# Performance work log

Hardware: AMD Instinct MI355X
Metric: run time of the kernel (lower is better)

## Reference

```python
import jax, jax.numpy as jnp
import numpy as np

D_MODEL = 1024
N_HEADS = 16
HEAD_DIM = D_MODEL // N_HEADS
D_FF = 4 * D_MODEL
EPS = 1e-5


def layer_norm(x, gamma, beta):
    mu = jnp.mean(x, axis=-1, keepdims=True)
    var = jnp.var(x, axis=-1, keepdims=True)
    return (x - mu) * jax.lax.rsqrt(var + EPS) * gamma + beta


def setup_inputs() -> dict:
    key = jax.random.key(0)
    ks = jax.random.split(key, 12)
    B, T, S = 4, 2048, 2048
    s_in = 1.0 / np.sqrt(D_MODEL)
    s_ff = 1.0 / np.sqrt(D_FF)
    return {
        "x": jax.random.normal(ks[0], (B, T, D_MODEL), jnp.float32),
        "context": jax.random.normal(ks[1], (B, S, D_MODEL), jnp.float32),
        "Wq": jax.random.normal(ks[2], (D_MODEL, D_MODEL), jnp.float32) * s_in,
        "Wk": jax.random.normal(ks[3], (D_MODEL, D_MODEL), jnp.float32) * s_in,
        "Wv": jax.random.normal(ks[4], (D_MODEL, D_MODEL), jnp.float32) * s_in,
        "Wo": jax.random.normal(ks[5], (D_MODEL, D_MODEL), jnp.float32) * s_in,
        "W1": jax.random.normal(ks[6], (D_FF, D_MODEL), jnp.float32) * s_in,
        "W2": jax.random.normal(ks[7], (D_MODEL, D_FF), jnp.float32) * s_ff,
        "g1": jnp.ones((D_MODEL,), jnp.float32),
        "b1": jnp.zeros((D_MODEL,), jnp.float32),
        "gc": jnp.ones((D_MODEL,), jnp.float32),
        "bc": jnp.zeros((D_MODEL,), jnp.float32),
        "g2": jnp.ones((D_MODEL,), jnp.float32),
        "b2": jnp.zeros((D_MODEL,), jnp.float32),
    }


def reference(x, context, Wq, Wk, Wv, Wo, W1, W2, g1, b1, gc, bc, g2, b2):
    B, T, C = x.shape
    S = context.shape[1]
    residual = x
    xn = layer_norm(x, g1, b1)
    cn = layer_norm(context, gc, bc)
    # torch Linear: y = x @ W.T ; split heads -> [B, H, T, Dh]
    q = (xn @ Wq.T).reshape(B, T, N_HEADS, HEAD_DIM).transpose(0, 2, 1, 3)
    k = (cn @ Wk.T).reshape(B, S, N_HEADS, HEAD_DIM).transpose(0, 2, 1, 3)
    v = (cn @ Wv.T).reshape(B, S, N_HEADS, HEAD_DIM).transpose(0, 2, 1, 3)
    scale = HEAD_DIM ** (-0.5)
    attn = jax.nn.softmax(jnp.einsum('bhtd,bhsd->bhts', q, k) * scale, axis=-1)
    o = jnp.einsum('bhts,bhsd->bhtd', attn, v).transpose(0, 2, 1, 3).reshape(B, T, C)
    x = residual + o @ Wo.T
    residual = x
    h = layer_norm(x, g2, b2)
    h = jax.nn.gelu(h @ W1.T, approximate=False) @ W2.T
    return residual + h
```

## Files before the change

kernel.cpp:

```cpp
#include <hip/hip_runtime.h>
#include <cstdint>
#include <cstddef>

typedef __attribute__((ext_vector_type(8))) short short8;
typedef __attribute__((ext_vector_type(4))) short short4v;
typedef __attribute__((ext_vector_type(4))) float f32x4;
typedef __attribute__((ext_vector_type(2))) unsigned uint2v;

#define DEV static __device__ __forceinline__

DEV short f2bf(float f) {
    unsigned u = __builtin_bit_cast(unsigned, f);
    unsigned r = (u + 0x7fffu + ((u >> 16) & 1u)) >> 16;
    return (short)r;
}

DEV unsigned cvt_pk_bf16(float a, float b) {
    unsigned r;
    asm("v_cvt_pk_bf16_f32 %0, %1, %2" : "=v"(r) : "v"(a), "v"(b));
    return r;
}

DEV float exp2_hw(float x) {
    float r;
    asm("v_exp_f32 %0, %1" : "=v"(r) : "v"(x));
    return r;
}

DEV void gld16(const void* g, void* l) {
    __builtin_amdgcn_global_load_lds((const __attribute__((address_space(1))) void*)g,
                                     (__attribute__((address_space(3))) void*)l, 16, 0, 0);
}

#define MFMA(c, a, b) asm volatile("v_mfma_f32_16x16x32_bf16 %0, %1, %2, %0" : "+v"(c) : "v"(a), "v"(b))
#define BAR() asm volatile("s_barrier" ::: "memory")

__global__ __launch_bounds__(256) void cvt_weights(
    const float* __restrict__ wq, const float* __restrict__ wk,
    const float* __restrict__ wv, const float* __restrict__ wo,
    const float* __restrict__ w1, const float* __restrict__ w2,
    short* __restrict__ dst) {
    long long gid = (long long)blockIdx.x * 256 + threadIdx.x;
    long long i4 = gid * 4;
    const float* src; long long loc;
    if (i4 < (4LL << 20)) {
        int s = (int)(i4 >> 20);
        src = (s == 0) ? wq : (s == 1) ? wk : (s == 2) ? wv : wo;
        loc = i4 & ((1LL << 20) - 1);
    } else {
        long long r = i4 - (4LL << 20);
        int s = (int)(r >> 22);
        src = s ? w2 : w1;
        loc = r & ((1LL << 22) - 1);
    }
    float4 v = *(const float4*)(src + loc);
    short4v o;
    o.x = f2bf(v.x); o.y = f2bf(v.y); o.z = f2bf(v.z); o.w = f2bf(v.w);
    *(short4v*)(dst + i4) = o;
}

__global__ __launch_bounds__(256) void ln_bf16(const float* __restrict__ x,
                                               const float* __restrict__ g,
                                               const float* __restrict__ bt,
                                               short* __restrict__ out) {
    int row = blockIdx.x;
    const float4* xr = (const float4*)(x + (size_t)row * 1024);
    float4 v = xr[threadIdx.x];
    float s  = v.x + v.y + v.z + v.w;
    float s2 = v.x*v.x + v.y*v.y + v.z*v.z + v.w*v.w;
    #pragma unroll
    for (int m = 1; m < 64; m <<= 1) { s += __shfl_xor(s, m); s2 += __shfl_xor(s2, m); }
    __shared__ float red[8];
    int wid = threadIdx.x >> 6;
    if ((threadIdx.x & 63) == 0) { red[wid] = s; red[4 + wid] = s2; }
    __syncthreads();
    s  = red[0] + red[1] + red[2] + red[3];
    s2 = red[4] + red[5] + red[6] + red[7];
    float mu  = s * (1.0f / 1024.0f);
    float var = fmaxf(s2 * (1.0f / 1024.0f) - mu * mu, 0.0f);
    float rs  = rsqrtf(var + 1e-5f);
    float4 gv = ((const float4*)g)[threadIdx.x];
    float4 bv = ((const float4*)bt)[threadIdx.x];
    short4v o;
    o.x = f2bf((v.x - mu) * rs * gv.x + bv.x);
    o.y = f2bf((v.y - mu) * rs * gv.y + bv.y);
    o.z = f2bf((v.z - mu) * rs * gv.z + bv.z);
    o.w = f2bf((v.w - mu) * rs * gv.w + bv.w);
    *(short4v*)(out + (size_t)row * 1024 + (size_t)threadIdx.x * 4) = o;
}

template<int MODE>
__global__ __launch_bounds__(256, 2) void gemm8(const short* __restrict__ A,
                                                const short* __restrict__ B,
                                                void* __restrict__ out,
                                                const float* __restrict__ resid,
                                                int M, int N, int K, float osc) {
    __shared__ short lds[3 * 12288];
    const int tid = threadIdx.x;
    const int nbn = N >> 7;
    int cpx = gridDim.x >> 3;
    int swz = (blockIdx.x & 7) * cpx + (blockIdx.x >> 3);
    int bm = swz / nbn, bn = swz % nbn;
    const int row0 = bm << 8, col0 = bn << 7;
    const int wid = tid >> 6, lane = tid & 63;
    const int wm = wid >> 1, wn = wid & 1;
    const int lr = lane & 15, lg = lane >> 4;

    auto stage = [&](int kt, int bb, int h) {
        const short* Ab = A + (size_t)row0 * K + kt * 32;
        const short* Bb = B + (size_t)col0 * K + kt * 32;
        #pragma unroll
        for (int l = 0; l < 2; ++l) {
            int g = (h * 2 + l) * 256 + tid;
            int r = g >> 2;
            int sl = (g & 3) ^ ((r >> 1) & 3);
            gld16(Ab + (size_t)r * K + sl * 8, &lds[bb + g * 8]);
        }
        {
            int g = h * 256 + tid;
            int r = g >> 2;
            int sl = (g & 3) ^ ((r >> 1) & 3);
            gld16(Bb + (size_t)r * K + sl * 8, &lds[bb + 8192 + g * 8]);
        }
    };

    f32x4 acc[8][4] = {};
    const int NK = K >> 5;

    stage(0, 0, 0);     stage(0, 0, 1);
    stage(1, 12288, 0); stage(1, 12288, 1);
    asm volatile("s_waitcnt vmcnt(6)" ::: "memory");
    BAR();

    int cb = 0, sb = 2;
    const int rsw = ((lr >> 1) & 3);
    short8 bfr[4];
    for (int kt = 0; kt < NK; ++kt) {
        int bb = cb * 12288, sbb = sb * 12288;
        bool st = (kt + 2) < NK;
        #pragma unroll
        for (int p = 0; p < 2; ++p) {
            short8 af[4];
            int csw = (lg ^ rsw) << 3;
            #pragma unroll
            for (int i = 0; i < 4; ++i)
                af[i] = *(const short8*)(lds + bb + (wm * 128 + (p * 4 + i) * 16 + lr) * 32 + csw);
            if (p == 0) {
                #pragma unroll
                for (int j = 0; j < 4; ++j)
                    bfr[j] = *(const short8*)(lds + bb + 8192 + (wn * 64 + j * 16 + lr) * 32 + csw);
            }
            if (st) stage(kt + 2, sbb, p);
            BAR();
            __builtin_amdgcn_s_setprio(1);
            #pragma unroll
            for (int i = 0; i < 4; ++i)
                #pragma unroll
                for (int j = 0; j < 4; ++j)
                    MFMA(acc[p * 4 + i][j], af[i], bfr[j]);
            __builtin_amdgcn_s_setprio(0);
            if (p == 1) {
                if (st) asm volatile("s_waitcnt vmcnt(6)" ::: "memory");
                else    asm volatile("s_waitcnt vmcnt(0)" ::: "memory");
            }
            BAR();
        }
        cb = (cb == 2) ? 0 : cb + 1;
        sb = (sb == 2) ? 0 : sb + 1;
    }
    asm volatile("s_nop 7\n\ts_nop 7");

    int orow0 = row0 + wm * 128, ocol0 = col0 + wn * 64;
    #pragma unroll
    for (int i = 0; i < 8; ++i)
        #pragma unroll
        for (int j = 0; j < 4; ++j)
            #pragma unroll
            for (int r = 0; r < 4; ++r) {
                int gr = orow0 + i * 16 + lg * 4 + r;
                int gc = ocol0 + j * 16 + lr;
                size_t off = (size_t)gr * N + gc;
                float v = acc[i][j][r];
                if constexpr (MODE == 0) {
                    ((short*)out)[off] = f2bf(v);
                } else if constexpr (MODE == 1) {
                    ((float*)out)[off] = v + resid[off];
                } else if constexpr (MODE == 2) {
                    float t = 0.5f * v * (1.0f + erff(v * 0.70710678118f));
                    ((short*)out)[off] = f2bf(t);
                } else {
                    ((short*)out)[off] = f2bf(v * osc);
                }
            }
}

__global__ __launch_bounds__(256) void attn(const short* __restrict__ Q,
                                            const short* __restrict__ K,
                                            const short* __restrict__ Vt,
                                            short* __restrict__ O) {
    __shared__ short lK[64 * 64];
    __shared__ short lV[64 * 64];
    __shared__ short lP[4][32 * 64];
    int tid = threadIdx.x;
    int qt = blockIdx.x & 15;
    int bh = blockIdx.x >> 4;
    int b = bh >> 4, h = bh & 15;
    int wid = tid >> 6, lane = tid & 63;
    int lr = lane & 15, lg = lane >> 4;
    int q0 = qt * 128 + wid * 32;

    short8 qf[2][2];
    #pragma unroll
    for (int fm = 0; fm < 2; ++fm)
        #pragma unroll
        for (int kb = 0; kb < 2; ++kb) {
            size_t roff = (size_t)(b * 2048 + q0 + fm * 16 + lr) * 1024 + h * 64 + kb * 32 + lg * 8;
            qf[fm][kb] = *(const short8*)(Q + roff);
        }

    f32x4 oacc[2][4] = {};
    float mrow[2] = { -1e30f, -1e30f };
    float lrs[2]  = { 0.0f, 0.0f };

    const short* Kb = K + (size_t)(b * 2048) * 1024 + h * 64;
    const short* Vb = Vt + (size_t)(h * 64) * 8192 + b * 2048;
    short* Pw = lP[wid];
    int albase = (lane & 48) >> 2;

    for (int st = 0; st < 32; ++st) {
        #pragma unroll
        for (int c = 0; c < 2; ++c) {
            int idx = c * 256 + tid;
            int r = idx >> 3, sp = idx & 7;
            int sl = sp ^ (r & 7);
            gld16(Kb + (size_t)(st * 64 + r) * 1024 + sl * 8, &lK[idx * 8]);
            gld16(Vb + (size_t)r * 8192 + st * 64 + sl * 8, &lV[idx * 8]);
        }
        __syncthreads();

        f32x4 sc2[4][2] = {};
        #pragma unroll
        for (int kb = 0; kb < 2; ++kb) {
            short8 kf[4];
            #pragma unroll
            for (int fn = 0; fn < 4; ++fn) {
                int kr = fn * 16 + lr;
                kf[fn] = *(const short8*)(lK + kr * 64 + (((kb * 4 + lg) ^ (kr & 7)) << 3));
            }
            #pragma unroll
            for (int fn = 0; fn < 4; ++fn)
                #pragma unroll
                for (int fm = 0; fm < 2; ++fm)
                    MFMA(sc2[fn][fm], kf[fn], qf[fm][kb]);
        }
        asm volatile("s_nop 7\n\ts_nop 7");

        #pragma unroll
        for (int fm = 0; fm < 2; ++fm) {
            float pm = sc2[0][fm][0];
            #pragma unroll
            for (int fn = 0; fn < 4; ++fn)
                #pragma unroll
                for (int r = 0; r < 4; ++r)
                    if (fn | r) pm = fmaxf(pm, sc2[fn][fm][r]);
            pm = fmaxf(pm, __shfl_xor(pm, 16));
            pm = fmaxf(pm, __shfl_xor(pm, 32));

            float mo = mrow[fm];
            float mn = mo;
            float al = 1.0f;
            if (!__all(pm <= mo + 8.0f)) {
                mn = fmaxf(mo, pm);
                al = exp2_hw(mo - mn);
                mrow[fm] = mn;
                #pragma unroll
                for (int r = 0; r < 4; ++r) {
                    float alr = __shfl(al, albase + r);
                    #pragma unroll
                    for (int fn = 0; fn < 4; ++fn) oacc[fm][fn][r] *= alr;
                }
            }

            float p[4][4];
            float ps = 0.0f;
            #pragma unroll
            for (int fn = 0; fn < 4; ++fn)
                #pragma unroll
                for (int r = 0; r < 4; ++r) {
                    p[fn][r] = exp2_hw(sc2[fn][fm][r] - mn);
                    ps += p[fn][r];
                }
            ps += __shfl_xor(ps, 16);
            ps += __shfl_xor(ps, 32);
            lrs[fm] = lrs[fm] * al + ps;

            int pr = fm * 16 + lr;
            int swz = (pr & 7) << 3;
            #pragma unroll
            for (int fn = 0; fn < 4; ++fn) {
                uint2v w;
                w.x = cvt_pk_bf16(p[fn][0], p[fn][1]);
                w.y = cvt_pk_bf16(p[fn][2], p[fn][3]);
                *(uint2v*)(Pw + ((pr * 64 + fn * 16 + lg * 4) ^ swz)) = w;
            }
        }

        #pragma unroll
        for (int kb = 0; kb < 2; ++kb) {
            short8 pa[2], vf[4];
            #pragma unroll
            for (int fm = 0; fm < 2; ++fm) {
                int pr = fm * 16 + lr;
                pa[fm] = *(const short8*)(Pw + pr * 64 + (((kb * 4 + lg) ^ (pr & 7)) << 3));
            }
            #pragma unroll
            for (int fn = 0; fn < 4; ++fn) {
                int vr = fn * 16 + lr;
                vf[fn] = *(const short8*)(lV + vr * 64 + (((kb * 4 + lg) ^ (vr & 7)) << 3));
            }
            #pragma unroll
            for (int fm = 0; fm < 2; ++fm)
                #pragma unroll
                for (int fn = 0; fn < 4; ++fn)
                    MFMA(oacc[fm][fn], pa[fm], vf[fn]);
        }
        __syncthreads();
    }
    asm volatile("s_nop 7\n\ts_nop 7");

    #pragma unroll
    for (int fm = 0; fm < 2; ++fm)
        #pragma unroll
        for (int r = 0; r < 4; ++r) {
            float linv = __shfl(lrs[fm], albase + r);
            float inv = 1.0f / linv;
            #pragma unroll
            for (int fn = 0; fn < 4; ++fn) {
                size_t off = (size_t)(b * 2048 + q0 + fm * 16 + lg * 4 + r) * 1024 + h * 64 + fn * 16 + lr;
                O[off] = f2bf(oacc[fm][fn][r] * inv);
            }
        }
}

extern "C" void kernel_launch(void* const* d_in, const int* in_sizes, int n_in,
                              void* d_out, int out_size, void* d_ws, size_t ws_size,
                              hipStream_t stream) {
    const float* x   = (const float*)d_in[0];
    const float* ctx = (const float*)d_in[1];
    const float* Wq  = (const float*)d_in[2];
    const float* Wk  = (const float*)d_in[3];
    const float* Wv  = (const float*)d_in[4];
    const float* Wo  = (const float*)d_in[5];
    const float* W1  = (const float*)d_in[6];
    const float* W2  = (const float*)d_in[7];
    const float* g1  = (const float*)d_in[8];
    const float* b1  = (const float*)d_in[9];
    const float* gc  = (const float*)d_in[10];
    const float* bc  = (const float*)d_in[11];
    const float* g2  = (const float*)d_in[12];
    const float* b2  = (const float*)d_in[13];

    char* ws = (char*)d_ws;
    const size_t OFF_W  = 0;
    const size_t OFF_XN = 25165824;
    const size_t OFF_CN = OFF_XN + 16777216;
    const size_t OFF_QB = OFF_CN + 16777216;
    const size_t OFF_KB = OFF_QB + 16777216;
    const size_t OFF_VT = OFF_KB + 16777216;
    const size_t OFF_X2 = OFF_VT + 16777216;
    const size_t OFF_F1 = OFF_X2 + 33554432;

    short* Wb = (short*)(ws + OFF_W);
    short* XN = (short*)(ws + OFF_XN);
    short* CN = (short*)(ws + OFF_CN);
    short* QB = (short*)(ws + OFF_QB);
    short* KB = (short*)(ws + OFF_KB);
    short* VT = (short*)(ws + OFF_VT);
    float* X2 = (float*)(ws + OFF_X2);
    short* F1 = (short*)(ws + OFF_F1);
    short* OB = XN;
    short* H  = CN;

    const size_t WQo = 0, WKo = 1048576, WVo = 2097152, WOo = 3145728;
    const size_t W1o = 4194304, W2o = 8388608;
    const float QSCALE = 0.125f * 1.4426950408889634f;

    cvt_weights<<<12288, 256, 0, stream>>>(Wq, Wk, Wv, Wo, W1, W2, Wb);
    ln_bf16<<<8192, 256, 0, stream>>>(x, g1, b1, XN);
    ln_bf16<<<8192, 256, 0, stream>>>(ctx, gc, bc, CN);
    gemm8<3><<<256, 256, 0, stream>>>(XN, Wb + WQo, QB, nullptr, 8192, 1024, 1024, QSCALE);
    gemm8<0><<<256, 256, 0, stream>>>(CN, Wb + WKo, KB, nullptr, 8192, 1024, 1024, 1.0f);
    gemm8<0><<<256, 256, 0, stream>>>(Wb + WVo, CN, VT, nullptr, 1024, 8192, 1024, 1.0f);
    attn<<<1024, 256, 0, stream>>>(QB, KB, VT, OB);
    gemm8<1><<<256, 256, 0, stream>>>(OB, Wb + WOo, X2, x, 8192, 1024, 1024, 1.0f);
    ln_bf16<<<8192, 256, 0, stream>>>(X2, g2, b2, H);
    gemm8<2><<<1024, 256, 0, stream>>>(H, Wb + W1o, F1, nullptr, 8192, 4096, 1024, 1.0f);
    gemm8<1><<<256, 256, 0, stream>>>(F1, Wb + W2o, (float*)d_out, X2, 8192, 1024, 4096, 1.0f);
}
```

Before: 474.8 us.

## Use 256x256 GEMM tiles, fuse QKV launches, split-K the FF2 GEMM

After: 490.4 us. 1.03x slower.

```diff
diff --git a/kernel.cpp b/kernel.cpp
--- a/kernel.cpp
+++ b/kernel.cpp
@@ -90,83 +90,134 @@
 }
 
 template<int MODE>
-__global__ __launch_bounds__(256, 2) void gemm8(const short* __restrict__ A,
-                                                const short* __restrict__ B,
-                                                void* __restrict__ out,
-                                                const float* __restrict__ resid,
-                                                int M, int N, int K, float osc) {
-    __shared__ short lds[3 * 12288];
+DEV void gemm_core(const short* __restrict__ A, const short* __restrict__ B,
+                   void* __restrict__ out, const float* __restrict__ resid,
+                   int N, int K, int lda, int ldb, float osc, int bm, int bn) {
+    __shared__ short lds[2 * 32768];
     const int tid = threadIdx.x;
-    const int nbn = N >> 7;
-    int cpx = gridDim.x >> 3;
-    int swz = (blockIdx.x & 7) * cpx + (blockIdx.x >> 3);
-    int bm = swz / nbn, bn = swz % nbn;
-    const int row0 = bm << 8, col0 = bn << 7;
+    const int row0 = bm << 8, col0 = bn << 8;
     const int wid = tid >> 6, lane = tid & 63;
-    const int wm = wid >> 1, wn = wid & 1;
+    const int wm = wid >> 2, wn = wid & 3;
     const int lr = lane & 15, lg = lane >> 4;
-
-    auto stage = [&](int kt, int bb, int h) {
-        const short* Ab = A + (size_t)row0 * K + kt * 32;
-        const short* Bb = B + (size_t)col0 * K + kt * 32;
+    const int NK = K >> 6;
+
+    auto stage = [&](int kt, int which) {
+        int d = kt & 1;
+        const short* src; int rb; int ld;
+        if (which < 2) { src = A; rb = row0; ld = lda; } else { src = B; rb = col0; ld = ldb; }
+        int rhalf = (which & 1) << 7;
+        short* dst = lds + d * 32768 + which * 8192;
         #pragma unroll
         for (int l = 0; l < 2; ++l) {
-            int g = (h * 2 + l) * 256 + tid;
-            int r = g >> 2;
-            int sl = (g & 3) ^ ((r >> 1) & 3);
-            gld16(Ab + (size_t)r * K + sl * 8, &lds[bb + g * 8]);
-        }
+            int g = l * 512 + tid;
+            int r = g >> 3, c = g & 7;
+            gld16(src + (size_t)(rb + rhalf + r) * ld + kt * 64 + ((c ^ (r & 7)) << 3),
+                  dst + g * 8);
+        }
+    };
+
+    f32x4 acc[8][4] = {};
+
+    stage(0, 0); stage(0, 1); stage(0, 2); stage(0, 3);
+    if (NK > 1) {
+        stage(1, 2); stage(1, 3);
+        asm volatile("s_waitcnt vmcnt(4)" ::: "memory");
+    } else {
+        asm volatile("s_waitcnt vmcnt(0)" ::: "memory");
+    }
+    BAR();
+
+    const int rBbase = (wn & 1) << 6;
+    for (int t = 0; t < NK; ++t) {
+        const short* bufA = lds + (t & 1) * 32768 + wm * 8192;
+        const short* bufB = lds + (t & 1) * 32768 + 16384 + (wn >> 1) * 8192;
+        bool st1 = (t + 1) < NK, st2 = (t + 2) < NK;
+        short8 bf2[2][4];
+
         {
-            int g = h * 256 + tid;
-            int r = g >> 2;
-            int sl = (g & 3) ^ ((r >> 1) & 3);
-            gld16(Bb + (size_t)r * K + sl * 8, &lds[bb + 8192 + g * 8]);
-        }
-    };
-
-    f32x4 acc[8][4] = {};
-    const int NK = K >> 5;
-
-    stage(0, 0, 0);     stage(0, 0, 1);
-    stage(1, 12288, 0); stage(1, 12288, 1);
-    asm volatile("s_waitcnt vmcnt(6)" ::: "memory");
-    BAR();
-
-    int cb = 0, sb = 2;
-    const int rsw = ((lr >> 1) & 3);
-    short8 bfr[4];
-    for (int kt = 0; kt < NK; ++kt) {
-        int bb = cb * 12288, sbb = sb * 12288;
-        bool st = (kt + 2) < NK;
-        #pragma unroll
-        for (int p = 0; p < 2; ++p) {
             short8 af[4];
-            int csw = (lg ^ rsw) << 3;
+            #pragma unroll
+            for (int i = 0; i < 4; ++i) {
+                int r = i * 16 + lr;
+                af[i] = *(const short8*)(bufA + r * 64 + ((lg ^ (r & 7)) << 3));
+            }
+            #pragma unroll
+            for (int j = 0; j < 4; ++j) {
+                int rB = rBbase + j * 16 + lr;
+                bf2[0][j] = *(const short8*)(bufB + rB * 64 + ((lg ^ (rB & 7)) << 3));
+            }
+            if (st1) stage(t + 1, 0);
+            BAR();
+            __builtin_amdgcn_s_setprio(1);
             #pragma unroll
             for (int i = 0; i < 4; ++i)
-                af[i] = *(const short8*)(lds + bb + (wm * 128 + (p * 4 + i) * 16 + lr) * 32 + csw);
-            if (p == 0) {
                 #pragma unroll
                 for (int j = 0; j < 4; ++j)
-                    bfr[j] = *(const short8*)(lds + bb + 8192 + (wn * 64 + j * 16 + lr) * 32 + csw);
-            }
-            if (st) stage(kt + 2, sbb, p);
+                    MFMA(acc[i][j], af[i], bf2[0][j]);
+            __builtin_amdgcn_s_setprio(0);
+            BAR();
+        }
+        {
+            short8 af[4];
+            #pragma unroll
+            for (int i = 0; i < 4; ++i) {
+                int r = i * 16 + lr;
+                af[i] = *(const short8*)(bufA + r * 64 + (((4 + lg) ^ (r & 7)) << 3));
+            }
+            #pragma unroll
+            for (int j = 0; j < 4; ++j) {
+                int rB = rBbase + j * 16 + lr;
+                bf2[1][j] = *(const short8*)(bufB + rB * 64 + (((4 + lg) ^ (rB & 7)) << 3));
+            }
+            if (st1) stage(t + 1, 1);
             BAR();
             __builtin_amdgcn_s_setprio(1);
             #pragma unroll
             for (int i = 0; i < 4; ++i)
                 #pragma unroll
                 for (int j = 0; j < 4; ++j)
-                    MFMA(acc[p * 4 + i][j], af[i], bfr[j]);
+                    MFMA(acc[i][j], af[i], bf2[1][j]);
             __builtin_amdgcn_s_setprio(0);
-            if (p == 1) {
-                if (st) asm volatile("s_waitcnt vmcnt(6)" ::: "memory");
-                else    asm volatile("s_waitcnt vmcnt(0)" ::: "memory");
-            }
-            BAR();
-        }
-        cb = (cb == 2) ? 0 : cb + 1;
-        sb = (sb == 2) ? 0 : sb + 1;
+            BAR();
+        }
+        {
+            short8 af[4];
+            #pragma unroll
+            for (int i = 0; i < 4; ++i) {
+                int r = 64 + i * 16 + lr;
+                af[i] = *(const short8*)(bufA + r * 64 + ((lg ^ (r & 7)) << 3));
+            }
+            if (st2) stage(t + 2, 2);
+            BAR();
+            __builtin_amdgcn_s_setprio(1);
+            #pragma unroll
+            for (int i = 0; i < 4; ++i)
+                #pragma unroll
+                for (int j = 0; j < 4; ++j)
+                    MFMA(acc[4 + i][j], af[i], bf2[0][j]);
+            __builtin_amdgcn_s_setprio(0);
+            BAR();
+        }
+        {
+            short8 af[4];
+            #pragma unroll
+            for (int i = 0; i < 4; ++i) {
+                int r = 64 + i * 16 + lr;
+                af[i] = *(const short8*)(bufA + r * 64 + (((4 + lg) ^ (r & 7)) << 3));
+            }
+            if (st2) stage(t + 2, 3);
+            BAR();
+            __builtin_amdgcn_s_setprio(1);
+            #pragma unroll
+            for (int i = 0; i < 4; ++i)
+                #pragma unroll
+                for (int j = 0; j < 4; ++j)
+                    MFMA(acc[4 + i][j], af[i], bf2[1][j]);
+            __builtin_amdgcn_s_setprio(0);
+            if (st2)      asm volatile("s_waitcnt vmcnt(4)" ::: "memory");
+            else if (st1) asm volatile("s_waitcnt vmcnt(0)" ::: "memory");
+            BAR();
+        }
     }
     asm volatile("s_nop 7\n\ts_nop 7");
 
@@ -181,17 +232,68 @@
                 int gc = ocol0 + j * 16 + lr;
                 size_t off = (size_t)gr * N + gc;
                 float v = acc[i][j][r];
-                if constexpr (MODE == 0) {
-                    ((short*)out)[off] = f2bf(v);
-                } else if constexpr (MODE == 1) {
-                    ((float*)out)[off] = v + resid[off];
+                if constexpr (MODE == 1) {
+                    ((float*)out)[off] = resid ? v + resid[off] : v;
                 } else if constexpr (MODE == 2) {
-                    float t = 0.5f * v * (1.0f + erff(v * 0.70710678118f));
-                    ((short*)out)[off] = f2bf(t);
+                    float tg = 0.5f * v * (1.0f + erff(v * 0.70710678118f));
+                    ((short*)out)[off] = f2bf(tg);
                 } else {
                     ((short*)out)[off] = f2bf(v * osc);
                 }
             }
+}
+
+__global__ __launch_bounds__(512, 2) void gemm_qkv(
+    const short* __restrict__ XN, const short* __restrict__ CN,
+    const short* __restrict__ Wq, const short* __restrict__ Wk, const short* __restrict__ Wv,
+    short* __restrict__ QB, short* __restrict__ KB, short* __restrict__ VT, float qscale) {
+    int sid = (blockIdx.x & 7) * 48 + (blockIdx.x >> 3);
+    int sub = sid >> 7, i = sid & 127;
+    const short *A, *B; short* o; float osc; int N, bm, bn;
+    if (sub == 0)      { A = XN; B = Wq; o = QB; osc = qscale; N = 1024; bm = i >> 2; bn = i & 3; }
+    else if (sub == 1) { A = CN; B = Wk; o = KB; osc = 1.0f;   N = 1024; bm = i >> 2; bn = i & 3; }
+    else               { A = Wv; B = CN; o = VT; osc = 1.0f;   N = 8192; bm = i >> 5; bn = i & 31; }
+    gemm_core<3>(A, B, o, nullptr, N, 1024, 1024, 1024, osc, bm, bn);
+}
+
+template<int MODE>
+__global__ __launch_bounds__(512, 2) void gemm_std(const short* __restrict__ A,
+                                                   const short* __restrict__ B,
+                                                   void* __restrict__ out,
+                                                   const float* __restrict__ resid,
+                                                   int N, int K, float osc) {
+    int cpx = gridDim.x >> 3;
+    int sid = (blockIdx.x & 7) * cpx + (blockIdx.x >> 3);
+    int nbn = N >> 8;
+    int bm = sid / nbn, bn = sid % nbn;
+    gemm_core<MODE>(A, B, out, resid, N, K, K, K, osc, bm, bn);
+}
+
+__global__ __launch_bounds__(512, 2) void gemm_ff2(const short* __restrict__ F1,
+                                                   const short* __restrict__ W2,
+                                                   float* __restrict__ dOut,
+                                                   float* __restrict__ P2,
+                                                   const float* __restrict__ X2) {
+    int sid = (blockIdx.x & 7) * 32 + (blockIdx.x >> 3);
+    int h = sid >> 7, i = sid & 127;
+    int bm = i >> 2, bn = i & 3;
+    const short* A = F1 + h * 2048;
+    const short* B = W2 + h * 2048;
+    float* o = h ? P2 : dOut;
+    const float* r = h ? nullptr : X2;
+    gemm_core<1>(A, B, o, r, 1024, 2048, 4096, 4096, 1.0f, bm, bn);
+}
+
+__global__ __launch_bounds__(256) void add_f32(float* __restrict__ dst,
+                                               const float* __restrict__ src, int n4) {
+    int i = blockIdx.x * 256 + threadIdx.x;
+    int stride = gridDim.x * 256;
+    for (; i < n4; i += stride) {
+        float4 a = ((const float4*)dst)[i];
+        float4 b = ((const float4*)src)[i];
+        a.x += b.x; a.y += b.y; a.z += b.z; a.w += b.w;
+        ((float4*)dst)[i] = a;
+    }
 }
 
 __global__ __launch_bounds__(256) void attn(const short* __restrict__ Q,
@@ -380,6 +482,7 @@
     short* F1 = (short*)(ws + OFF_F1);
     short* OB = XN;
     short* H  = CN;
+    float* P2 = (float*)(ws + OFF_QB);
 
     const size_t WQo = 0, WKo = 1048576, WVo = 2097152, WOo = 3145728;
     const size_t W1o = 4194304, W2o = 8388608;
@@ -388,12 +491,11 @@
     cvt_weights<<<12288, 256, 0, stream>>>(Wq, Wk, Wv, Wo, W1, W2, Wb);
     ln_bf16<<<8192, 256, 0, stream>>>(x, g1, b1, XN);
     ln_bf16<<<8192, 256, 0, stream>>>(ctx, gc, bc, CN);
-    gemm8<3><<<256, 256, 0, stream>>>(XN, Wb + WQo, QB, nullptr, 8192, 1024, 1024, QSCALE);
-    gemm8<0><<<256, 256, 0, stream>>>(CN, Wb + WKo, KB, nullptr, 8192, 1024, 1024, 1.0f);
-    gemm8<0><<<256, 256, 0, stream>>>(Wb + WVo, CN, VT, nullptr, 1024, 8192, 1024, 1.0f);
+    gemm_qkv<<<384, 512, 0, stream>>>(XN, CN, Wb + WQo, Wb + WKo, Wb + WVo, QB, KB, VT, QSCALE);
     attn<<<1024, 256, 0, stream>>>(QB, KB, VT, OB);
-    gemm8<1><<<256, 256, 0, stream>>>(OB, Wb + WOo, X2, x, 8192, 1024, 1024, 1.0f);
+    gemm_std<1><<<128, 512, 0, stream>>>(OB, Wb + WOo, X2, x, 1024, 1024, 1.0f);
     ln_bf16<<<8192, 256, 0, stream>>>(X2, g2, b2, H);
-    gemm8<2><<<1024, 256, 0, stream>>>(H, Wb + W1o, F1, nullptr, 8192, 4096, 1024, 1.0f);
-    gemm8<1><<<256, 256, 0, stream>>>(F1, Wb + W2o, (float*)d_out, X2, 8192, 1024, 4096, 1.0f);
-}
+    gemm_std<2><<<512, 512, 0, stream>>>(H, Wb + W1o, F1, nullptr, 4096, 1024, 1.0f);
+    gemm_ff2<<<256, 512, 0, stream>>>(F1, Wb + W2o, (float*)d_out, P2, X2);
+    add_f32<<<2048, 256, 0, stream>>>((float*)d_out, P2, 2097152);
+}
```
